# Performance work log

Hardware: AMD Instinct MI355X
Metric: run time of the kernel (lower is better)

The kernel has to match this reference:

```python
import jax, jax.numpy as jnp
import numpy as np

N = 100000   # nodes
E = 600000   # edges
DIN = 128
H = 128
DOUT = 64
EPS = 1e-5   # BatchNorm1d default eps


def setup_inputs() -> dict:
    key = jax.random.key(0)
    ks = jax.random.split(key, 16)
    w = lambda k, shape: jax.random.normal(k, shape, jnp.float32) * 0.05
    return {
        "x": jax.random.normal(ks[0], (N, DIN), jnp.float32),
        "edge_index": jax.random.randint(ks[1], (2, E), 0, N),
        # layer 1: SAGEConv(DIN -> H)  (lin_l on aggregated neighbors w/ bias, lin_r on root)
        "Wl1": w(ks[2], (DIN, H)), "bl1": jnp.zeros((H,), jnp.float32), "Wr1": w(ks[3], (DIN, H)),
        "g1": jnp.ones((H,), jnp.float32), "be1": jnp.zeros((H,), jnp.float32),
        "rm1": jax.random.normal(ks[4], (H,), jnp.float32) * 0.1,
        "rv1": jax.random.uniform(ks[5], (H,), jnp.float32, 0.5, 1.5),
        # layer 2: SAGEConv(H -> H)
        "Wl2": w(ks[6], (H, H)), "bl2": jnp.zeros((H,), jnp.float32), "Wr2": w(ks[7], (H, H)),
        "g2": jnp.ones((H,), jnp.float32), "be2": jnp.zeros((H,), jnp.float32),
        "rm2": jax.random.normal(ks[8], (H,), jnp.float32) * 0.1,
        "rv2": jax.random.uniform(ks[9], (H,), jnp.float32, 0.5, 1.5),
        # layer 3: SAGEConv(H -> DOUT), no BN/ReLU after
        "Wl3": w(ks[10], (H, DOUT)), "bl3": jnp.zeros((DOUT,), jnp.float32), "Wr3": w(ks[11], (H, DOUT)),
    }


def _sage_conv(x, src, dst, Wl, bl, Wr):
    # mean-aggregate source features at targets, then lin_l(agg) + b + lin_r(x)
    agg = jax.ops.segment_sum(x[src], dst, num_segments=N)          # [N, d]
    deg = jax.ops.segment_sum(jnp.ones((src.shape[0],), x.dtype), dst, num_segments=N)
    agg = agg / jnp.maximum(deg, 1.0)[:, None]
    return agg @ Wl + bl + x @ Wr


def _bn_eval(h, g, b, rm, rv):
    return (h - rm) * (g * jax.lax.rsqrt(rv + EPS)) + b


def reference(x, edge_index, Wl1, bl1, Wr1, g1, be1, rm1, rv1,
              Wl2, bl2, Wr2, g2, be2, rm2, rv2, Wl3, bl3, Wr3):
    src, dst = edge_index[0], edge_index[1]
    h = jax.nn.relu(_bn_eval(_sage_conv(x, src, dst, Wl1, bl1, Wr1), g1, be1, rm1, rv1))
    h = jax.nn.relu(_bn_eval(_sage_conv(h, src, dst, Wl2, bl2, Wr2), g2, be2, rm2, rv2))
    return _sage_conv(h, src, dst, Wl3, bl3, Wr3)   # [N, DOUT]
```

## Files before the change

kernel.cpp:

```cpp
#include <hip/hip_runtime.h>

#define CAP 48

typedef short  s8v  __attribute__((ext_vector_type(8)));
typedef float  f4v  __attribute__((ext_vector_type(4)));

__device__ __forceinline__ unsigned short f2bf(float f) {
    unsigned u = __float_as_uint(f);
    u += 0x7FFFu + ((u >> 16) & 1u);
    return (unsigned short)(u >> 16);
}
__device__ __forceinline__ float bflo(unsigned v) { return __uint_as_float(v << 16); }
__device__ __forceinline__ float bfhi(unsigned v) { return __uint_as_float(v & 0xffff0000u); }

__global__ __launch_bounds__(256) void k_bucket(const int* __restrict__ src, const int* __restrict__ dst,
                                                int E, int* __restrict__ cnt, int* __restrict__ bucket) {
    int e = blockIdx.x * 256 + threadIdx.x;
    if (e < E) {
        int d = dst[e];
        int slot = atomicAdd(&cnt[d], 1);
        if (slot < CAP) bucket[(size_t)d * CAP + slot] = src[e];
    }
}

__global__ __launch_bounds__(256) void k_prepack(const float* W0, const float* W1, const float* W2,
                                                 const float* W3, const float* W4, const float* W5,
                                                 unsigned short* P0, unsigned short* P1, unsigned short* P2,
                                                 unsigned short* P3, unsigned short* P4, unsigned short* P5,
                                                 const float* g1, const float* be1, const float* rm1, const float* rv1, const float* bl1,
                                                 const float* g2, const float* be2, const float* rm2, const float* rv2, const float* bl2,
                                                 float* P) {
    if (blockIdx.y == 6) {
        if (blockIdx.x == 0 && threadIdx.x < 128) {
            int j = threadIdx.x;
            float s1 = g1[j] * rsqrtf(rv1[j] + 1e-5f);
            P[j]       = s1;
            P[128 + j] = (bl1[j] - rm1[j]) * s1 + be1[j];
            float s2 = g2[j] * rsqrtf(rv2[j] + 1e-5f);
            P[256 + j] = s2;
            P[384 + j] = (bl2[j] - rm2[j]) * s2 + be2[j];
        }
        return;
    }
    const float* W; unsigned short* Pk; int JD;
    switch (blockIdx.y) {
        case 0: W = W0; Pk = P0; JD = 128; break;
        case 1: W = W1; Pk = P1; JD = 128; break;
        case 2: W = W2; Pk = P2; JD = 128; break;
        case 3: W = W3; Pk = P3; JD = 128; break;
        case 4: W = W4; Pk = P4; JD = 64;  break;
        default:W = W5; Pk = P5; JD = 64;  break;
    }
    int o = blockIdx.x * 256 + threadIdx.x;
    if (o >= 128 * JD) return;
    int j    = o & 7;
    int lane = (o >> 3) & 63;
    int t    = o >> 9;
    int nt   = t % (JD / 16);
    int kt   = t / (JD / 16);
    int k = kt * 32 + (lane >> 4) * 8 + j;
    int n = nt * 16 + (lane & 15);
    Pk[o] = f2bf(W[(size_t)k * JD + n]);
}

__global__ __launch_bounds__(256) void k_cvt(const float* __restrict__ in, unsigned short* __restrict__ out, int n4) {
    int i = blockIdx.x * 256 + threadIdx.x;
    if (i < n4) {
        float4 v = ((const float4*)in)[i];
        ushort4 o;
        o.x = f2bf(v.x); o.y = f2bf(v.y); o.z = f2bf(v.z); o.w = f2bf(v.w);
        ((ushort4*)out)[i] = o;
    }
}

template<bool T3>
__global__ __launch_bounds__(256) void k_fused(const unsigned short* __restrict__ feat,
                                               const int* __restrict__ cnt, const int* __restrict__ bucket,
                                               const unsigned short* __restrict__ Bl, const unsigned short* __restrict__ Br,
                                               const float* __restrict__ scale, const float* __restrict__ shift,
                                               unsigned short* __restrict__ out,
                                               const unsigned short* __restrict__ W3p, unsigned short* __restrict__ t3,
                                               int n) {
    __shared__ unsigned short sA[32 * 136];
    __shared__ unsigned short sH[T3 ? 32 * 136 : 8];
    const int tid  = threadIdx.x;
    const int wave = tid >> 6;
    const int lane = tid & 63;
    const int nb0  = blockIdx.x * 32;
    if (nb0 >= n) return;

    {
        const int g  = lane >> 5;
        const int li = lane & 31;
        const uint2* inp = (const uint2*)feat;
        const int base = g << 5;
        #pragma unroll
        for (int p = 0; p < 4; p++) {
            int row  = wave * 8 + p * 2 + g;
            int node = nb0 + row;
            if (node < n) {
                int c = cnt[node]; if (c > CAP) c = CAP;
                int idxv = 0;
                if (li < c) idxv = bucket[(size_t)node * CAP + li];
                float a0 = 0.f, a1 = 0.f, a2 = 0.f, a3 = 0.f;
                int cc = c < 32 ? c : 32;
                int s = 0;
                for (; s + 4 <= cc; s += 4) {
                    int i0 = __shfl(idxv, base + s);
                    int i1 = __shfl(idxv, base + s + 1);
                    int i2 = __shfl(idxv, base + s + 2);
                    int i3 = __shfl(idxv, base + s + 3);
                    uint2 v0 = inp[(size_t)i0 * 32 + li];
                    uint2 v1 = inp[(size_t)i1 * 32 + li];
                    uint2 v2 = inp[(size_t)i2 * 32 + li];
                    uint2 v3 = inp[(size_t)i3 * 32 + li];
                    a0 += bflo(v0.x) + bflo(v1.x) + bflo(v2.x) + bflo(v3.x);
                    a1 += bfhi(v0.x) + bfhi(v1.x) + bfhi(v2.x) + bfhi(v3.x);
                    a2 += bflo(v0.y) + bflo(v1.y) + bflo(v2.y) + bflo(v3.y);
                    a3 += bfhi(v0.y) + bfhi(v1.y) + bfhi(v2.y) + bfhi(v3.y);
                }
                for (; s < cc; s++) {
                    int i0 = __shfl(idxv, base + s);
                    uint2 v0 = inp[(size_t)i0 * 32 + li];
                    a0 += bflo(v0.x); a1 += bfhi(v0.x); a2 += bflo(v0.y); a3 += bfhi(v0.y);
                }
                for (; s < c; s++) {
                    int i0 = bucket[(size_t)node * CAP + s];
                    uint2 v0 = inp[(size_t)i0 * 32 + li];
                    a0 += bflo(v0.x); a1 += bfhi(v0.x); a2 += bflo(v0.y); a3 += bfhi(v0.y);
                }
                float iv = 1.0f / fmaxf((float)c, 1.0f);
                uint2 o;
                o.x = (unsigned)f2bf(a0 * iv) | ((unsigned)f2bf(a1 * iv) << 16);
                o.y = (unsigned)f2bf(a2 * iv) | ((unsigned)f2bf(a3 * iv) << 16);
                ((uint2*)(sA + row * 136))[li] = o;
            }
        }
    }
    __syncthreads();

    const int m = lane & 15;
    const int q = lane >> 4;
    const int nt0 = wave * 2;
    const int rg0 = min(nb0 + m,      n - 1);
    const int rg1 = min(nb0 + 16 + m, n - 1);

    f4v acc[2][2];
    #pragma unroll
    for (int mt = 0; mt < 2; mt++)
        #pragma unroll
        for (int c = 0; c < 2; c++) {
            acc[mt][c][0] = 0.f; acc[mt][c][1] = 0.f; acc[mt][c][2] = 0.f; acc[mt][c][3] = 0.f;
        }

    #pragma unroll
    for (int kt = 0; kt < 4; kt++) {
        const int ko = kt * 32 + q * 8;
        s8v a0 = *(const s8v*)(sA + m * 136 + ko);
        s8v a1 = *(const s8v*)(sA + (16 + m) * 136 + ko);
        s8v a0d = *(const s8v*)(feat + (size_t)rg0 * 128 + ko);
        s8v a1d = *(const s8v*)(feat + (size_t)rg1 * 128 + ko);
        #pragma unroll
        for (int c = 0; c < 2; c++) {
            s8v b  = *(const s8v*)(Bl + ((size_t)(kt * 8 + nt0 + c) * 64 + lane) * 8);
            acc[0][c] = __builtin_amdgcn_mfma_f32_16x16x32_bf16(a0, b, acc[0][c], 0, 0, 0);
            acc[1][c] = __builtin_amdgcn_mfma_f32_16x16x32_bf16(a1, b, acc[1][c], 0, 0, 0);
            s8v b2 = *(const s8v*)(Br + ((size_t)(kt * 8 + nt0 + c) * 64 + lane) * 8);
            acc[0][c] = __builtin_amdgcn_mfma_f32_16x16x32_bf16(a0d, b2, acc[0][c], 0, 0, 0);
            acc[1][c] = __builtin_amdgcn_mfma_f32_16x16x32_bf16(a1d, b2, acc[1][c], 0, 0, 0);
        }
    }

    float scv[2], shv[2];
    #pragma unroll
    for (int c = 0; c < 2; c++) {
        int col = (nt0 + c) * 16 + m;
        scv[c] = scale[col]; shv[c] = shift[col];
    }
    #pragma unroll
    for (int mt = 0; mt < 2; mt++) {
        #pragma unroll
        for (int reg = 0; reg < 4; reg++) {
            int rloc = mt * 16 + q * 4 + reg;
            int row  = nb0 + rloc;
            if (row < n) {
                #pragma unroll
                for (int c = 0; c < 2; c++) {
                    int col = (nt0 + c) * 16 + m;
                    float v = fmaxf(acc[mt][c][reg] * scv[c] + shv[c], 0.f);
                    unsigned short u = f2bf(v);
                    out[(size_t)row * 128 + col] = u;
                    if constexpr (T3) sH[rloc * 136 + col] = u;
                }
            }
        }
    }

    if constexpr (T3) {
        __syncthreads();
        f4v a3c[2];
        #pragma unroll
        for (int mt = 0; mt < 2; mt++) { a3c[mt][0] = 0.f; a3c[mt][1] = 0.f; a3c[mt][2] = 0.f; a3c[mt][3] = 0.f; }
        #pragma unroll
        for (int kt = 0; kt < 4; kt++) {
            const int ko = kt * 32 + q * 8;
            s8v a0 = *(const s8v*)(sH + m * 136 + ko);
            s8v a1 = *(const s8v*)(sH + (16 + m) * 136 + ko);
            s8v b  = *(const s8v*)(W3p + ((size_t)(kt * 4 + wave) * 64 + lane) * 8);
            a3c[0] = __builtin_amdgcn_mfma_f32_16x16x32_bf16(a0, b, a3c[0], 0, 0, 0);
            a3c[1] = __builtin_amdgcn_mfma_f32_16x16x32_bf16(a1, b, a3c[1], 0, 0, 0);
        }
        #pragma unroll
        for (int mt = 0; mt < 2; mt++) {
            #pragma unroll
            for (int reg = 0; reg < 4; reg++) {
                int row = nb0 + mt * 16 + q * 4 + reg;
                if (row < n) t3[(size_t)row * 64 + wave * 16 + m] = f2bf(a3c[mt][reg]);
            }
        }
    }
}

__global__ __launch_bounds__(256) void k_final(const unsigned short* __restrict__ hb2,
                                               const unsigned short* __restrict__ t3,
                                               const int* __restrict__ cnt, const int* __restrict__ bucket,
                                               const unsigned short* __restrict__ Bp, const float* __restrict__ bias,
                                               float* __restrict__ outf, int n) {
    __shared__ float sG[32 * 68];
    const int tid  = threadIdx.x;
    const int wave = tid >> 6;
    const int lane = tid & 63;
    const int nb0  = blockIdx.x * 32;
    if (nb0 >= n) return;

    {
        const int g  = lane >> 4;
        const int li = lane & 15;
        const uint2* inp = (const uint2*)t3;
        const int base = g << 4;
        #pragma unroll
        for (int p = 0; p < 2; p++) {
            int row  = wave * 8 + p * 4 + g;
            int node = nb0 + row;
            if (node < n) {
                int c = cnt[node]; if (c > CAP) c = CAP;
                int idxv = 0;
                if (li < c) idxv = bucket[(size_t)node * CAP + li];
                float a0 = 0.f, a1 = 0.f, a2 = 0.f, a3 = 0.f;
                int cc = c < 16 ? c : 16;
                int s = 0;
                for (; s + 4 <= cc; s += 4) {
                    int i0 = __shfl(idxv, base + s);
                    int i1 = __shfl(idxv, base + s + 1);
                    int i2 = __shfl(idxv, base + s + 2);
                    int i3 = __shfl(idxv, base + s + 3);
                    uint2 v0 = inp[(size_t)i0 * 16 + li];
                    uint2 v1 = inp[(size_t)i1 * 16 + li];
                    uint2 v2 = inp[(size_t)i2 * 16 + li];
                    uint2 v3 = inp[(size_t)i3 * 16 + li];
                    a0 += bflo(v0.x) + bflo(v1.x) + bflo(v2.x) + bflo(v3.x);
                    a1 += bfhi(v0.x) + bfhi(v1.x) + bfhi(v2.x) + bfhi(v3.x);
                    a2 += bflo(v0.y) + bflo(v1.y) + bflo(v2.y) + bflo(v3.y);
                    a3 += bfhi(v0.y) + bfhi(v1.y) + bfhi(v2.y) + bfhi(v3.y);
                }
                for (; s < cc; s++) {
                    int i0 = __shfl(idxv, base + s);
                    uint2 v0 = inp[(size_t)i0 * 16 + li];
                    a0 += bflo(v0.x); a1 += bfhi(v0.x); a2 += bflo(v0.y); a3 += bfhi(v0.y);
                }
                for (; s < c; s++) {
                    int i0 = bucket[(size_t)node * CAP + s];
                    uint2 v0 = inp[(size_t)i0 * 16 + li];
                    a0 += bflo(v0.x); a1 += bfhi(v0.x); a2 += bflo(v0.y); a3 += bfhi(v0.y);
                }
                float iv = 1.0f / fmaxf((float)c, 1.0f);
                float4 o; o.x = a0 * iv; o.y = a1 * iv; o.z = a2 * iv; o.w = a3 * iv;
                ((float4*)(sG + row * 68))[li] = o;
            }
        }
    }
    __syncthreads();

    const int m = lane & 15;
    const int q = lane >> 4;
    const int rg0 = min(nb0 + m,      n - 1);
    const int rg1 = min(nb0 + 16 + m, n - 1);

    f4v acc[2];
    #pragma unroll
    for (int mt = 0; mt < 2; mt++) { acc[mt][0] = 0.f; acc[mt][1] = 0.f; acc[mt][2] = 0.f; acc[mt][3] = 0.f; }

    #pragma unroll
    for (int kt = 0; kt < 4; kt++) {
        const int ko = kt * 32 + q * 8;
        s8v a0 = *(const s8v*)(hb2 + (size_t)rg0 * 128 + ko);
        s8v a1 = *(const s8v*)(hb2 + (size_t)rg1 * 128 + ko);
        s8v b  = *(const s8v*)(Bp + ((size_t)(kt * 4 + wave) * 64 + lane) * 8);
        acc[0] = __builtin_amdgcn_mfma_f32_16x16x32_bf16(a0, b, acc[0], 0, 0, 0);
        acc[1] = __builtin_amdgcn_mfma_f32_16x16x32_bf16(a1, b, acc[1], 0, 0, 0);
    }

    const int col = wave * 16 + m;
    const float bv = bias[col];
    #pragma unroll
    for (int mt = 0; mt < 2; mt++) {
        #pragma unroll
        for (int reg = 0; reg < 4; reg++) {
            int rloc = mt * 16 + q * 4 + reg;
            int row  = nb0 + rloc;
            if (row < n) outf[(size_t)row * 64 + col] = acc[mt][reg] + sG[rloc * 68 + col] + bv;
        }
    }
}

extern "C" void kernel_launch(void* const* d_in, const int* in_sizes, int n_in,
                              void* d_out, int out_size, void* d_ws, size_t ws_size,
                              hipStream_t stream) {
    const float* x   = (const float*)d_in[0];
    const int*   ei  = (const int*)d_in[1];
    const float* Wl1 = (const float*)d_in[2];
    const float* bl1 = (const float*)d_in[3];
    const float* Wr1 = (const float*)d_in[4];
    const float* g1  = (const float*)d_in[5];
    const float* be1 = (const float*)d_in[6];
    const float* rm1 = (const float*)d_in[7];
    const float* rv1 = (const float*)d_in[8];
    const float* Wl2 = (const float*)d_in[9];
    const float* bl2 = (const float*)d_in[10];
    const float* Wr2 = (const float*)d_in[11];
    const float* g2  = (const float*)d_in[12];
    const float* be2 = (const float*)d_in[13];
    const float* rm2 = (const float*)d_in[14];
    const float* rv2 = (const float*)d_in[15];
    const float* Wl3 = (const float*)d_in[16];
    const float* bl3 = (const float*)d_in[17];
    const float* Wr3 = (const float*)d_in[18];

    const int N = in_sizes[0] / 128;
    const int E = in_sizes[1] / 2;
    const int* src = ei;
    const int* dst = ei + E;

    char* w = (char*)d_ws;
    auto au = [](size_t v) { return (v + 1023) & ~(size_t)1023; };
    size_t off = 0;
    int*            cnt    = (int*)(w + off);            off += au((size_t)N * 4);
    int*            bucket = (int*)(w + off);            off += au((size_t)N * CAP * 4);
    unsigned short* xb     = (unsigned short*)(w + off); off += au((size_t)N * 128 * 2);
    unsigned short* hb     = (unsigned short*)(w + off); off += au((size_t)N * 128 * 2);
    unsigned short* hb2    = (unsigned short*)(w + off); off += au((size_t)N * 128 * 2);
    unsigned short* t3b    = (unsigned short*)(w + off); off += au((size_t)N * 64 * 2);
    unsigned short* Wp[6];
    Wp[0] = (unsigned short*)(w + off); off += au(128 * 128 * 2);
    Wp[1] = (unsigned short*)(w + off); off += au(128 * 128 * 2);
    Wp[2] = (unsigned short*)(w + off); off += au(128 * 128 * 2);
    Wp[3] = (unsigned short*)(w + off); off += au(128 * 128 * 2);
    Wp[4] = (unsigned short*)(w + off); off += au(128 * 64 * 2);
    Wp[5] = (unsigned short*)(w + off); off += au(128 * 64 * 2);
    float* P = (float*)(w + off); off += 2048;
    (void)ws_size; (void)n_in;

    hipMemsetAsync(cnt, 0, (size_t)N * 4, stream);
    k_bucket<<<(E + 255) / 256, 256, 0, stream>>>(src, dst, E, cnt, bucket);
    dim3 pg(64, 7);
    k_prepack<<<pg, 256, 0, stream>>>(Wl1, Wr1, Wl2, Wr2, Wl3, Wr3,
                                      Wp[0], Wp[1], Wp[2], Wp[3], Wp[4], Wp[5],
                                      g1, be1, rm1, rv1, bl1, g2, be2, rm2, rv2, bl2, P);
    k_cvt<<<((N * 128 / 4) + 255) / 256, 256, 0, stream>>>(x, xb, N * 128 / 4);

    const int grid = (N + 31) / 32;

    k_fused<false><<<grid, 256, 0, stream>>>(xb, cnt, bucket, Wp[0], Wp[1],
                                             P, P + 128, hb, nullptr, nullptr, N);
    k_fused<true><<<grid, 256, 0, stream>>>(hb, cnt, bucket, Wp[2], Wp[3],
                                            P + 256, P + 384, hb2, Wp[4], t3b, N);
    k_final<<<grid, 256, 0, stream>>>(hb2, t3b, cnt, bucket, Wp[5], bl3, (float*)d_out, N);
}
```

Before: 296.3 us.

## Use 16-byte gathers with zero-row padding for branchless neighbor aggregation

Neighbor gathers in both fused and final kernels now load uint4 (8 bf16) per lane instead of uint2. Fewer lanes cover each row, so more rows are processed per wave. Invalid neighbor slots point at an extra zeroed sentinel row N in each feature buffer, so the first 8 or 16 loads are fully unrolled without per-edge bounds checks. This aims to raise memory-level parallelism and cut instruction overhead, at the cost of wasted loads of the zero row when degree is low, plus extra workspace.

```diff
diff --git a/kernel.cpp b/kernel.cpp
--- a/kernel.cpp
+++ b/kernel.cpp
@@ -12,6 +12,9 @@
 }
 __device__ __forceinline__ float bflo(unsigned v) { return __uint_as_float(v << 16); }
 __device__ __forceinline__ float bfhi(unsigned v) { return __uint_as_float(v & 0xffff0000u); }
+
+#define ACC8(v)  do { a[0]+=bflo((v).x); a[1]+=bfhi((v).x); a[2]+=bflo((v).y); a[3]+=bfhi((v).y); \
+                      a[4]+=bflo((v).z); a[5]+=bfhi((v).z); a[6]+=bflo((v).w); a[7]+=bfhi((v).w); } while(0)
 
 __global__ __launch_bounds__(256) void k_bucket(const int* __restrict__ src, const int* __restrict__ dst,
                                                 int E, int* __restrict__ cnt, int* __restrict__ bucket) {
@@ -29,16 +32,24 @@
                                                  unsigned short* P3, unsigned short* P4, unsigned short* P5,
                                                  const float* g1, const float* be1, const float* rm1, const float* rv1, const float* bl1,
                                                  const float* g2, const float* be2, const float* rm2, const float* rv2, const float* bl2,
-                                                 float* P) {
+                                                 float* P,
+                                                 unsigned short* xb, unsigned short* hb, unsigned short* hb2,
+                                                 unsigned short* t3b, int N) {
     if (blockIdx.y == 6) {
-        if (blockIdx.x == 0 && threadIdx.x < 128) {
-            int j = threadIdx.x;
-            float s1 = g1[j] * rsqrtf(rv1[j] + 1e-5f);
-            P[j]       = s1;
-            P[128 + j] = (bl1[j] - rm1[j]) * s1 + be1[j];
-            float s2 = g2[j] * rsqrtf(rv2[j] + 1e-5f);
-            P[256 + j] = s2;
-            P[384 + j] = (bl2[j] - rm2[j]) * s2 + be2[j];
+        if (blockIdx.x == 0) {
+            int i = threadIdx.x;
+            if (i < 128) {
+                float s1 = g1[i] * rsqrtf(rv1[i] + 1e-5f);
+                P[i]       = s1;
+                P[128 + i] = (bl1[i] - rm1[i]) * s1 + be1[i];
+                float s2 = g2[i] * rsqrtf(rv2[i] + 1e-5f);
+                P[256 + i] = s2;
+                P[384 + i] = (bl2[i] - rm2[i]) * s2 + be2[i];
+                xb [(size_t)N * 128 + i] = 0;
+                hb [(size_t)N * 128 + i] = 0;
+                hb2[(size_t)N * 128 + i] = 0;
+                if (i < 64) t3b[(size_t)N * 64 + i] = 0;
+            }
         }
         return;
     }
@@ -90,50 +101,54 @@
     if (nb0 >= n) return;
 
     {
-        const int g  = lane >> 5;
-        const int li = lane & 31;
-        const uint2* inp = (const uint2*)feat;
-        const int base = g << 5;
-        #pragma unroll
-        for (int p = 0; p < 4; p++) {
-            int row  = wave * 8 + p * 2 + g;
-            int node = nb0 + row;
+        const int q4   = lane >> 4;
+        const int li   = lane & 15;
+        const int base = q4 << 4;
+        const uint4* inp = (const uint4*)feat;
+        int rows[2], cs[2], idxs[2];
+        #pragma unroll
+        for (int t = 0; t < 2; t++) {
+            rows[t] = wave * 8 + t * 4 + q4;
+            int node = nb0 + rows[t];
+            bool ok = node < n;
+            int c = ok ? cnt[node] : 0; if (c > CAP) c = CAP;
+            cs[t] = c;
+            idxs[t] = (ok && li < c) ? bucket[(size_t)node * CAP + li] : n;
+        }
+        #pragma unroll
+        for (int t = 0; t < 2; t++) {
+            const int c = cs[t];
+            float a[8] = {0.f, 0.f, 0.f, 0.f, 0.f, 0.f, 0.f, 0.f};
+            if (c > 0) {
+                #pragma unroll
+                for (int u = 0; u < 8; u++) {
+                    int idx = __shfl(idxs[t], base + u);
+                    uint4 v = inp[(size_t)idx * 16 + li];
+                    ACC8(v);
+                }
+            }
+            if (c > 8) {
+                #pragma unroll
+                for (int u = 8; u < 16; u++) {
+                    int idx = __shfl(idxs[t], base + u);
+                    uint4 v = inp[(size_t)idx * 16 + li];
+                    ACC8(v);
+                }
+            }
+            const int node = nb0 + rows[t];
+            for (int s = 16; s < c; s++) {
+                int idx = bucket[(size_t)node * CAP + s];
+                uint4 v = inp[(size_t)idx * 16 + li];
+                ACC8(v);
+            }
             if (node < n) {
-                int c = cnt[node]; if (c > CAP) c = CAP;
-                int idxv = 0;
-                if (li < c) idxv = bucket[(size_t)node * CAP + li];
-                float a0 = 0.f, a1 = 0.f, a2 = 0.f, a3 = 0.f;
-                int cc = c < 32 ? c : 32;
-                int s = 0;
-                for (; s + 4 <= cc; s += 4) {
-                    int i0 = __shfl(idxv, base + s);
-                    int i1 = __shfl(idxv, base + s + 1);
-                    int i2 = __shfl(idxv, base + s + 2);
-                    int i3 = __shfl(idxv, base + s + 3);
-                    uint2 v0 = inp[(size_t)i0 * 32 + li];
-                    uint2 v1 = inp[(size_t)i1 * 32 + li];
-                    uint2 v2 = inp[(size_t)i2 * 32 + li];
-                    uint2 v3 = inp[(size_t)i3 * 32 + li];
-                    a0 += bflo(v0.x) + bflo(v1.x) + bflo(v2.x) + bflo(v3.x);
-                    a1 += bfhi(v0.x) + bfhi(v1.x) + bfhi(v2.x) + bfhi(v3.x);
-                    a2 += bflo(v0.y) + bflo(v1.y) + bflo(v2.y) + bflo(v3.y);
-                    a3 += bfhi(v0.y) + bfhi(v1.y) + bfhi(v2.y) + bfhi(v3.y);
-                }
-                for (; s < cc; s++) {
-                    int i0 = __shfl(idxv, base + s);
-                    uint2 v0 = inp[(size_t)i0 * 32 + li];
-                    a0 += bflo(v0.x); a1 += bfhi(v0.x); a2 += bflo(v0.y); a3 += bfhi(v0.y);
-                }
-                for (; s < c; s++) {
-                    int i0 = bucket[(size_t)node * CAP + s];
-                    uint2 v0 = inp[(size_t)i0 * 32 + li];
-                    a0 += bflo(v0.x); a1 += bfhi(v0.x); a2 += bflo(v0.y); a3 += bfhi(v0.y);
-                }
                 float iv = 1.0f / fmaxf((float)c, 1.0f);
-                uint2 o;
-                o.x = (unsigned)f2bf(a0 * iv) | ((unsigned)f2bf(a1 * iv) << 16);
-                o.y = (unsigned)f2bf(a2 * iv) | ((unsigned)f2bf(a3 * iv) << 16);
-                ((uint2*)(sA + row * 136))[li] = o;
+                uint4 o;
+                o.x = (unsigned)f2bf(a[0] * iv) | ((unsigned)f2bf(a[1] * iv) << 16);
+                o.y = (unsigned)f2bf(a[2] * iv) | ((unsigned)f2bf(a[3] * iv) << 16);
+                o.z = (unsigned)f2bf(a[4] * iv) | ((unsigned)f2bf(a[5] * iv) << 16);
+                o.w = (unsigned)f2bf(a[6] * iv) | ((unsigned)f2bf(a[7] * iv) << 16);
+                *(uint4*)(sA + rows[t] * 136 + li * 8) = o;
             }
         }
     }
@@ -234,49 +249,44 @@
     if (nb0 >= n) return;
 
     {
-        const int g  = lane >> 4;
-        const int li = lane & 15;
-        const uint2* inp = (const uint2*)t3;
-        const int base = g << 4;
-        #pragma unroll
-        for (int p = 0; p < 2; p++) {
-            int row  = wave * 8 + p * 4 + g;
-            int node = nb0 + row;
-            if (node < n) {
-                int c = cnt[node]; if (c > CAP) c = CAP;
-                int idxv = 0;
-                if (li < c) idxv = bucket[(size_t)node * CAP + li];
-                float a0 = 0.f, a1 = 0.f, a2 = 0.f, a3 = 0.f;
-                int cc = c < 16 ? c : 16;
-                int s = 0;
-                for (; s + 4 <= cc; s += 4) {
-                    int i0 = __shfl(idxv, base + s);
-                    int i1 = __shfl(idxv, base + s + 1);
-                    int i2 = __shfl(idxv, base + s + 2);
-                    int i3 = __shfl(idxv, base + s + 3);
-                    uint2 v0 = inp[(size_t)i0 * 16 + li];
-                    uint2 v1 = inp[(size_t)i1 * 16 + li];
-                    uint2 v2 = inp[(size_t)i2 * 16 + li];
-                    uint2 v3 = inp[(size_t)i3 * 16 + li];
-                    a0 += bflo(v0.x) + bflo(v1.x) + bflo(v2.x) + bflo(v3.x);
-                    a1 += bfhi(v0.x) + bfhi(v1.x) + bfhi(v2.x) + bfhi(v3.x);
-                    a2 += bflo(v0.y) + bflo(v1.y) + bflo(v2.y) + bflo(v3.y);
-                    a3 += bfhi(v0.y) + bfhi(v1.y) + bfhi(v2.y) + bfhi(v3.y);
-                }
-                for (; s < cc; s++) {
-                    int i0 = __shfl(idxv, base + s);
-                    uint2 v0 = inp[(size_t)i0 * 16 + li];
-                    a0 += bflo(v0.x); a1 += bfhi(v0.x); a2 += bflo(v0.y); a3 += bfhi(v0.y);
-                }
-                for (; s < c; s++) {
-                    int i0 = bucket[(size_t)node * CAP + s];
-                    uint2 v0 = inp[(size_t)i0 * 16 + li];
-                    a0 += bflo(v0.x); a1 += bfhi(v0.x); a2 += bflo(v0.y); a3 += bfhi(v0.y);
-                }
-                float iv = 1.0f / fmaxf((float)c, 1.0f);
-                float4 o; o.x = a0 * iv; o.y = a1 * iv; o.z = a2 * iv; o.w = a3 * iv;
-                ((float4*)(sG + row * 68))[li] = o;
-            }
+        const int e8   = lane >> 3;
+        const int li   = lane & 7;
+        const int base = e8 << 3;
+        const uint4* inp = (const uint4*)t3;
+        const int row  = wave * 8 + e8;
+        const int node = nb0 + row;
+        const bool ok  = node < n;
+        int c = ok ? cnt[node] : 0; if (c > CAP) c = CAP;
+        int idx1 = (ok && li < c)     ? bucket[(size_t)node * CAP + li]     : n;
+        int idx2 = (ok && li + 8 < c) ? bucket[(size_t)node * CAP + li + 8] : n;
+        float a[8] = {0.f, 0.f, 0.f, 0.f, 0.f, 0.f, 0.f, 0.f};
+        if (c > 0) {
+            #pragma unroll
+            for (int u = 0; u < 8; u++) {
+                int idx = __shfl(idx1, base + u);
+                uint4 v = inp[(size_t)idx * 8 + li];
+                ACC8(v);
+            }
+        }
+        if (c > 8) {
+            #pragma unroll
+            for (int u = 0; u < 8; u++) {
+                int idx = __shfl(idx2, base + u);
+                uint4 v = inp[(size_t)idx * 8 + li];
+                ACC8(v);
+            }
+        }
+        for (int s = 16; s < c; s++) {
+            int idx = bucket[(size_t)node * CAP + s];
+            uint4 v = inp[(size_t)idx * 8 + li];
+            ACC8(v);
+        }
+        if (ok) {
+            float iv = 1.0f / fmaxf((float)c, 1.0f);
+            float4 o1; o1.x = a[0] * iv; o1.y = a[1] * iv; o1.z = a[2] * iv; o1.w = a[3] * iv;
+            float4 o2; o2.x = a[4] * iv; o2.y = a[5] * iv; o2.z = a[6] * iv; o2.w = a[7] * iv;
+            *(float4*)(sG + row * 68 + li * 8)     = o1;
+            *(float4*)(sG + row * 68 + li * 8 + 4) = o2;
         }
     }
     __syncthreads();
@@ -346,10 +356,10 @@
     size_t off = 0;
     int*            cnt    = (int*)(w + off);            off += au((size_t)N * 4);
     int*            bucket = (int*)(w + off);            off += au((size_t)N * CAP * 4);
-    unsigned short* xb     = (unsigned short*)(w + off); off += au((size_t)N * 128 * 2);
-    unsigned short* hb     = (unsigned short*)(w + off); off += au((size_t)N * 128 * 2);
-    unsigned short* hb2    = (unsigned short*)(w + off); off += au((size_t)N * 128 * 2);
-    unsigned short* t3b    = (unsigned short*)(w + off); off += au((size_t)N * 64 * 2);
+    unsigned short* xb     = (unsigned short*)(w + off); off += au((size_t)(N + 1) * 128 * 2);
+    unsigned short* hb     = (unsigned short*)(w + off); off += au((size_t)(N + 1) * 128 * 2);
+    unsigned short* hb2    = (unsigned short*)(w + off); off += au((size_t)(N + 1) * 128 * 2);
+    unsigned short* t3b    = (unsigned short*)(w + off); off += au((size_t)(N + 1) * 64 * 2);
     unsigned short* Wp[6];
     Wp[0] = (unsigned short*)(w + off); off += au(128 * 128 * 2);
     Wp[1] = (unsigned short*)(w + off); off += au(128 * 128 * 2);
@@ -365,7 +375,8 @@
     dim3 pg(64, 7);
     k_prepack<<<pg, 256, 0, stream>>>(Wl1, Wr1, Wl2, Wr2, Wl3, Wr3,
                                       Wp[0], Wp[1], Wp[2], Wp[3], Wp[4], Wp[5],
-                                      g1, be1, rm1, rv1, bl1, g2, be2, rm2, rv2, bl2, P);
+                                      g1, be1, rm1, rv1, bl1, g2, be2, rm2, rv2, bl2, P,
+                                      xb, hb, hb2, t3b, N);
     k_cvt<<<((N * 128 / 4) + 255) / 256, 256, 0, stream>>>(x, xb, N * 128 / 4);
 
     const int grid = (N + 31) / 32;
```

Result: no change. 293.4 us (-1.0%).

## Replace pull-based neighbor gather with push-based packed bf16 atomic scatter

Applied to the files above, without the earlier changes.

Aggregation is restructured from a per-destination gather inside the fused dense kernels to a separate push kernel. Each source node scatters its degree-normalised features to its destinations using packed bf16 atomic adds into zeroed accumulators, and the dense kernels then read those accumulators from global memory. This is meant to replace the gather's random reads with coalesced per-source reads. In exchange it adds extra kernels, memsets, accumulator round trips and heavy atomic traffic, and accumulating in bf16 loses precision and makes results order-dependent.

```diff
diff --git a/kernel.cpp b/kernel.cpp
--- a/kernel.cpp
+++ b/kernel.cpp
@@ -1,4 +1,5 @@
 #include <hip/hip_runtime.h>
+#include <hip/hip_bf16.h>
 
 #define CAP 48
 
@@ -12,15 +13,39 @@
 }
 __device__ __forceinline__ float bflo(unsigned v) { return __uint_as_float(v << 16); }
 __device__ __forceinline__ float bfhi(unsigned v) { return __uint_as_float(v & 0xffff0000u); }
-
-__global__ __launch_bounds__(256) void k_bucket(const int* __restrict__ src, const int* __restrict__ dst,
-                                                int E, int* __restrict__ cnt, int* __restrict__ bucket) {
+__device__ __forceinline__ float bf2f(unsigned short b) { return __uint_as_float(((unsigned)b) << 16); }
+
+__device__ __forceinline__ void atomic_pk_bf16(unsigned* p, unsigned v) {
+#if __has_builtin(__builtin_amdgcn_global_atomic_fadd_v2bf16)
+    typedef short s2v __attribute__((ext_vector_type(2)));
+    __builtin_amdgcn_global_atomic_fadd_v2bf16((s2v*)p, *(s2v*)&v);
+#else
+    unsigned old = *p, assumed;
+    do {
+        assumed = old;
+        unsigned nv = (unsigned)f2bf(bflo(assumed) + bflo(v)) |
+                      ((unsigned)f2bf(bfhi(assumed) ? bfhi(assumed) + bfhi(v) : bfhi(v)) << 16);
+        nv = (unsigned)f2bf(bflo(assumed) + bflo(v)) | ((unsigned)f2bf(bfhi(assumed) + bfhi(v)) << 16);
+        old = atomicCAS(p, assumed, nv);
+    } while (old != assumed);
+#endif
+}
+
+__global__ __launch_bounds__(256) void k_csr(const int* __restrict__ src, const int* __restrict__ dst,
+                                             int E, int* __restrict__ cntS, int* __restrict__ cntD,
+                                             int* __restrict__ bucketS) {
     int e = blockIdx.x * 256 + threadIdx.x;
     if (e < E) {
-        int d = dst[e];
-        int slot = atomicAdd(&cnt[d], 1);
-        if (slot < CAP) bucket[(size_t)d * CAP + slot] = src[e];
-    }
+        int s = src[e], d = dst[e];
+        int slot = atomicAdd(&cntS[s], 1);
+        if (slot < CAP) bucketS[(size_t)s * CAP + slot] = d;
+        atomicAdd(&cntD[d], 1);
+    }
+}
+
+__global__ __launch_bounds__(256) void k_invdeg(const int* __restrict__ cntD, float* __restrict__ invdeg, int n) {
+    int i = blockIdx.x * 256 + threadIdx.x;
+    if (i < n) invdeg[i] = 1.0f / fmaxf((float)cntD[i], 1.0f);
 }
 
 __global__ __launch_bounds__(256) void k_prepack(const float* W0, const float* W1, const float* W2,
@@ -32,13 +57,13 @@
                                                  float* P) {
     if (blockIdx.y == 6) {
         if (blockIdx.x == 0 && threadIdx.x < 128) {
-            int j = threadIdx.x;
-            float s1 = g1[j] * rsqrtf(rv1[j] + 1e-5f);
-            P[j]       = s1;
-            P[128 + j] = (bl1[j] - rm1[j]) * s1 + be1[j];
-            float s2 = g2[j] * rsqrtf(rv2[j] + 1e-5f);
-            P[256 + j] = s2;
-            P[384 + j] = (bl2[j] - rm2[j]) * s2 + be2[j];
+            int i = threadIdx.x;
+            float s1 = g1[i] * rsqrtf(rv1[i] + 1e-5f);
+            P[i]       = s1;
+            P[128 + i] = (bl1[i] - rm1[i]) * s1 + be1[i];
+            float s2 = g2[i] * rsqrtf(rv2[i] + 1e-5f);
+            P[256 + i] = s2;
+            P[384 + i] = (bl2[i] - rm2[i]) * s2 + be2[i];
         }
         return;
     }
@@ -73,15 +98,40 @@
     }
 }
 
+template<int DW>
+__global__ __launch_bounds__(256) void k_push(const unsigned* __restrict__ feat, const int* __restrict__ cntS,
+                                              const int* __restrict__ bucketS, const float* __restrict__ invdeg,
+                                              unsigned* __restrict__ acc, int n) {
+    int wv   = (blockIdx.x * 256 + threadIdx.x) >> 6;
+    int lane = threadIdx.x & 63;
+    if (wv >= n) return;
+    int c = cntS[wv]; if (c > CAP) c = CAP;
+    if (c == 0) return;
+    int   dl = bucketS[(size_t)wv * CAP + (lane < CAP ? lane : CAP - 1)];
+    float il = (lane < c) ? invdeg[dl] : 0.f;
+    float fx = 0.f, fy = 0.f;
+    if (lane < DW) {
+        unsigned rv = feat[(size_t)wv * DW + lane];
+        fx = bflo(rv); fy = bfhi(rv);
+    }
+    for (int s = 0; s < c; s++) {
+        int   d  = __shfl(dl, s);
+        float iv = __shfl(il, s);
+        if (lane < DW) {
+            unsigned pv = (unsigned)f2bf(fx * iv) | ((unsigned)f2bf(fy * iv) << 16);
+            atomic_pk_bf16(acc + (size_t)d * DW + lane, pv);
+        }
+    }
+}
+
 template<bool T3>
-__global__ __launch_bounds__(256) void k_fused(const unsigned short* __restrict__ feat,
-                                               const int* __restrict__ cnt, const int* __restrict__ bucket,
+__global__ __launch_bounds__(256) void k_dense(const unsigned short* __restrict__ accm,
+                                               const unsigned short* __restrict__ feat,
                                                const unsigned short* __restrict__ Bl, const unsigned short* __restrict__ Br,
                                                const float* __restrict__ scale, const float* __restrict__ shift,
                                                unsigned short* __restrict__ out,
                                                const unsigned short* __restrict__ W3p, unsigned short* __restrict__ t3,
                                                int n) {
-    __shared__ unsigned short sA[32 * 136];
     __shared__ unsigned short sH[T3 ? 32 * 136 : 8];
     const int tid  = threadIdx.x;
     const int wave = tid >> 6;
@@ -89,56 +139,6 @@
     const int nb0  = blockIdx.x * 32;
     if (nb0 >= n) return;
 
-    {
-        const int g  = lane >> 5;
-        const int li = lane & 31;
-        const uint2* inp = (const uint2*)feat;
-        const int base = g << 5;
-        #pragma unroll
-        for (int p = 0; p < 4; p++) {
-            int row  = wave * 8 + p * 2 + g;
-            int node = nb0 + row;
-            if (node < n) {
-                int c = cnt[node]; if (c > CAP) c = CAP;
-                int idxv = 0;
-                if (li < c) idxv = bucket[(size_t)node * CAP + li];
-                float a0 = 0.f, a1 = 0.f, a2 = 0.f, a3 = 0.f;
-                int cc = c < 32 ? c : 32;
-                int s = 0;
-                for (; s + 4 <= cc; s += 4) {
-                    int i0 = __shfl(idxv, base + s);
-                    int i1 = __shfl(idxv, base + s + 1);
-                    int i2 = __shfl(idxv, base + s + 2);
-                    int i3 = __shfl(idxv, base + s + 3);
-                    uint2 v0 = inp[(size_t)i0 * 32 + li];
-                    uint2 v1 = inp[(size_t)i1 * 32 + li];
-                    uint2 v2 = inp[(size_t)i2 * 32 + li];
-                    uint2 v3 = inp[(size_t)i3 * 32 + li];
-                    a0 += bflo(v0.x) + bflo(v1.x) + bflo(v2.x) + bflo(v3.x);
-                    a1 += bfhi(v0.x) + bfhi(v1.x) + bfhi(v2.x) + bfhi(v3.x);
-                    a2 += bflo(v0.y) + bflo(v1.y) + bflo(v2.y) + bflo(v3.y);
-                    a3 += bfhi(v0.y) + bfhi(v1.y) + bfhi(v2.y) + bfhi(v3.y);
-                }
-                for (; s < cc; s++) {
-                    int i0 = __shfl(idxv, base + s);
-                    uint2 v0 = inp[(size_t)i0 * 32 + li];
-                    a0 += bflo(v0.x); a1 += bfhi(v0.x); a2 += bflo(v0.y); a3 += bfhi(v0.y);
-                }
-                for (; s < c; s++) {
-                    int i0 = bucket[(size_t)node * CAP + s];
-                    uint2 v0 = inp[(size_t)i0 * 32 + li];
-                    a0 += bflo(v0.x); a1 += bfhi(v0.x); a2 += bflo(v0.y); a3 += bfhi(v0.y);
-                }
-                float iv = 1.0f / fmaxf((float)c, 1.0f);
-                uint2 o;
-                o.x = (unsigned)f2bf(a0 * iv) | ((unsigned)f2bf(a1 * iv) << 16);
-                o.y = (unsigned)f2bf(a2 * iv) | ((unsigned)f2bf(a3 * iv) << 16);
-                ((uint2*)(sA + row * 136))[li] = o;
-            }
-        }
-    }
-    __syncthreads();
-
     const int m = lane & 15;
     const int q = lane >> 4;
     const int nt0 = wave * 2;
@@ -156,8 +156,8 @@
     #pragma unroll
     for (int kt = 0; kt < 4; kt++) {
         const int ko = kt * 32 + q * 8;
-        s8v a0 = *(const s8v*)(sA + m * 136 + ko);
-        s8v a1 = *(const s8v*)(sA + (16 + m) * 136 + ko);
+        s8v a0  = *(const s8v*)(accm + (size_t)rg0 * 128 + ko);
+        s8v a1  = *(const s8v*)(accm + (size_t)rg1 * 128 + ko);
         s8v a0d = *(const s8v*)(feat + (size_t)rg0 * 128 + ko);
         s8v a1d = *(const s8v*)(feat + (size_t)rg1 * 128 + ko);
         #pragma unroll
@@ -222,64 +222,14 @@
 }
 
 __global__ __launch_bounds__(256) void k_final(const unsigned short* __restrict__ hb2,
-                                               const unsigned short* __restrict__ t3,
-                                               const int* __restrict__ cnt, const int* __restrict__ bucket,
+                                               const unsigned short* __restrict__ acc3,
                                                const unsigned short* __restrict__ Bp, const float* __restrict__ bias,
                                                float* __restrict__ outf, int n) {
-    __shared__ float sG[32 * 68];
     const int tid  = threadIdx.x;
     const int wave = tid >> 6;
     const int lane = tid & 63;
     const int nb0  = blockIdx.x * 32;
     if (nb0 >= n) return;
-
-    {
-        const int g  = lane >> 4;
-        const int li = lane & 15;
-        const uint2* inp = (const uint2*)t3;
-        const int base = g << 4;
-        #pragma unroll
-        for (int p = 0; p < 2; p++) {
-            int row  = wave * 8 + p * 4 + g;
-            int node = nb0 + row;
-            if (node < n) {
-                int c = cnt[node]; if (c > CAP) c = CAP;
-                int idxv = 0;
-                if (li < c) idxv = bucket[(size_t)node * CAP + li];
-                float a0 = 0.f, a1 = 0.f, a2 = 0.f, a3 = 0.f;
-                int cc = c < 16 ? c : 16;
-                int s = 0;
-                for (; s + 4 <= cc; s += 4) {
-                    int i0 = __shfl(idxv, base + s);
-                    int i1 = __shfl(idxv, base + s + 1);
-                    int i2 = __shfl(idxv, base + s + 2);
-                    int i3 = __shfl(idxv, base + s + 3);
-                    uint2 v0 = inp[(size_t)i0 * 16 + li];
-                    uint2 v1 = inp[(size_t)i1 * 16 + li];
-                    uint2 v2 = inp[(size_t)i2 * 16 + li];
-                    uint2 v3 = inp[(size_t)i3 * 16 + li];
-                    a0 += bflo(v0.x) + bflo(v1.x) + bflo(v2.x) + bflo(v3.x);
-                    a1 += bfhi(v0.x) + bfhi(v1.x) + bfhi(v2.x) + bfhi(v3.x);
-                    a2 += bflo(v0.y) + bflo(v1.y) + bflo(v2.y) + bflo(v3.y);
-                    a3 += bfhi(v0.y) + bfhi(v1.y) + bfhi(v2.y) + bfhi(v3.y);
-                }
-                for (; s < cc; s++) {
-                    int i0 = __shfl(idxv, base + s);
-                    uint2 v0 = inp[(size_t)i0 * 16 + li];
-                    a0 += bflo(v0.x); a1 += bfhi(v0.x); a2 += bflo(v0.y); a3 += bfhi(v0.y);
-                }
-                for (; s < c; s++) {
-                    int i0 = bucket[(size_t)node * CAP + s];
-                    uint2 v0 = inp[(size_t)i0 * 16 + li];
-                    a0 += bflo(v0.x); a1 += bfhi(v0.x); a2 += bflo(v0.y); a3 += bfhi(v0.y);
-                }
-                float iv = 1.0f / fmaxf((float)c, 1.0f);
-                float4 o; o.x = a0 * iv; o.y = a1 * iv; o.z = a2 * iv; o.w = a3 * iv;
-                ((float4*)(sG + row * 68))[li] = o;
-            }
-        }
-    }
-    __syncthreads();
 
     const int m = lane & 15;
     const int q = lane >> 4;
@@ -308,7 +258,8 @@
         for (int reg = 0; reg < 4; reg++) {
             int rloc = mt * 16 + q * 4 + reg;
             int row  = nb0 + rloc;
-            if (row < n) outf[(size_t)row * 64 + col] = acc[mt][reg] + sG[rloc * 68 + col] + bv;
+            if (row < n)
+                outf[(size_t)row * 64 + col] = acc[mt][reg] + bf2f(acc3[(size_t)row * 64 + col]) + bv;
         }
     }
 }
@@ -344,12 +295,17 @@
     char* w = (char*)d_ws;
     auto au = [](size_t v) { return (v + 1023) & ~(size_t)1023; };
     size_t off = 0;
-    int*            cnt    = (int*)(w + off);            off += au((size_t)N * 4);
-    int*            bucket = (int*)(w + off);            off += au((size_t)N * CAP * 4);
+    int*            cntS   = (int*)(w + off);            off += (size_t)N * 4;
+    int*            cntD   = (int*)(w + off);            off += au((size_t)N * 4);
+    float*          invdeg = (float*)(w + off);          off += au((size_t)N * 4);
+    int*            bucketS= (int*)(w + off);            off += au((size_t)N * CAP * 4);
     unsigned short* xb     = (unsigned short*)(w + off); off += au((size_t)N * 128 * 2);
     unsigned short* hb     = (unsigned short*)(w + off); off += au((size_t)N * 128 * 2);
     unsigned short* hb2    = (unsigned short*)(w + off); off += au((size_t)N * 128 * 2);
     unsigned short* t3b    = (unsigned short*)(w + off); off += au((size_t)N * 64 * 2);
+    unsigned short* acc1   = (unsigned short*)(w + off); off += (size_t)N * 128 * 2;
+    unsigned short* acc2   = (unsigned short*)(w + off); off += (size_t)N * 128 * 2;
+    unsigned short* acc3   = (unsigned short*)(w + off); off += au((size_t)N * 64 * 2);
     unsigned short* Wp[6];
     Wp[0] = (unsigned short*)(w + off); off += au(128 * 128 * 2);
     Wp[1] = (unsigned short*)(w + off); off += au(128 * 128 * 2);
@@ -360,19 +316,25 @@
     float* P = (float*)(w + off); off += 2048;
     (void)ws_size; (void)n_in;
 
-    hipMemsetAsync(cnt, 0, (size_t)N * 4, stream);
-    k_bucket<<<(E + 255) / 256, 256, 0, stream>>>(src, dst, E, cnt, bucket);
+    hipMemsetAsync(cntS, 0, (size_t)N * 8, stream);
+    hipMemsetAsync(acc1, 0, (size_t)N * (128 + 128 + 64) * 2, stream);
+    k_csr<<<(E + 255) / 256, 256, 0, stream>>>(src, dst, E, cntS, cntD, bucketS);
+    k_invdeg<<<(N + 255) / 256, 256, 0, stream>>>(cntD, invdeg, N);
     dim3 pg(64, 7);
     k_prepack<<<pg, 256, 0, stream>>>(Wl1, Wr1, Wl2, Wr2, Wl3, Wr3,
                                       Wp[0], Wp[1], Wp[2], Wp[3], Wp[4], Wp[5],
                                       g1, be1, rm1, rv1, bl1, g2, be2, rm2, rv2, bl2, P);
     k_cvt<<<((N * 128 / 4) + 255) / 256, 256, 0, stream>>>(x, xb, N * 128 / 4);
 
-    const int grid = (N + 31) / 32;
-
-    k_fused<false><<<grid, 256, 0, stream>>>(xb, cnt, bucket, Wp[0], Wp[1],
-                                             P, P + 128, hb, nullptr, nullptr, N);
-    k_fused<true><<<grid, 256, 0, stream>>>(hb, cnt, bucket, Wp[2], Wp[3],
-                                            P + 256, P + 384, hb2, Wp[4], t3b, N);
-    k_final<<<grid, 256, 0, stream>>>(hb2, t3b, cnt, bucket, Wp[5], bl3, (float*)d_out, N);
-}
+    const int pushGrid  = ((size_t)N * 64 + 255) / 256;
+    const int denseGrid = (N + 31) / 32;
+
+    k_push<64><<<pushGrid, 256, 0, stream>>>((const unsigned*)xb, cntS, bucketS, invdeg, (unsigned*)acc1, N);
+    k_dense<false><<<denseGrid, 256, 0, stream>>>(acc1, xb, Wp[0], Wp[1], P, P + 128, hb, nullptr, nullptr, N);
+
+    k_push<64><<<pushGrid, 256, 0, stream>>>((const unsigned*)hb, cntS, bucketS, invdeg, (unsigned*)acc2, N);
+    k_dense<true><<<denseGrid, 256, 0, stream>>>(acc2, hb, Wp[2], Wp[3], P + 256, P + 384, hb2, Wp[4], t3b, N);
+
+    k_push<32><<<pushGrid, 256, 0, stream>>>((const unsigned*)t3b, cntS, bucketS, invdeg, (unsigned*)acc3, N);
+    k_final<<<denseGrid, 256, 0, stream>>>(hb2, acc3, Wp[5], bl3, (float*)d_out, N);
+}
```

Measured after the change: 597.2 us. +101.5%, slower.
